# Performance work log

Hardware: AMD Instinct MI355X
Metric: run time of the kernel (lower is better)

## Reference

```python
import jax
import jax.numpy as jnp
import numpy as np

EPS = 1e-06


def _topk_mask(scores, k):
    # scores: (T, E); hard top-k mask along last dim
    _, idx = jax.lax.top_k(scores, k)            # (T, k)
    hard = jax.nn.one_hot(idx, scores.shape[-1]).sum(axis=-2)  # (T, E)
    return hard.astype(bool)


def setup_inputs() -> dict:
    key = jax.random.key(0)
    k1, k2, k3 = jax.random.split(key, 3)
    T, D, E = 8192, 4096, 64
    h_td = jax.random.normal(k1, (T, D), dtype=jnp.float32)
    # eqx.nn.Linear weight layout: (out_features, in_features)
    W = jax.random.normal(k2, (E, D), dtype=jnp.float32) * (1.0 / np.sqrt(D))
    bias_e = jax.random.normal(k3, (E,), dtype=jnp.float32)
    return {"h_td": h_td, "W": W, "bias_e": bias_e, "k": 8}


def reference(h_td, W, bias_e, k):
    # Linear(d_model -> E), no bias in proj; external bias_e added after
    logits_te = jnp.einsum("td,ed->te", h_td, W) + bias_e[None, :]  # (T, E)
    # Soft combine weights always from clean logits
    weight_te = jax.nn.softmax(logits_te, axis=-1)
    # Training path: Gumbel noise on the selection scores only
    gkey = jax.random.key(42)
    u = jax.random.uniform(gkey, logits_te.shape, minval=EPS, maxval=1.0 - EPS)
    g = -jnp.log(-jnp.log(u))
    sel_scores = logits_te + g
    mask_te = _topk_mask(sel_scores, k)
    return (mask_te, weight_te, logits_te)
```

## Files before the change

### kernel.cpp

```cpp
#include <hip/hip_runtime.h>
#include <stdint.h>
#include <math.h>

#define T_DIM 8192
#define D_DIM 4096
#define E_DIM 64
#define TE (T_DIM * E_DIM)
#define GAP_MARGIN 4e-3
#define BK 256
#define NCHUNK (D_DIM / BK)
#define KSTEPS (BK / 32)

typedef __attribute__((ext_vector_type(8))) short short8_t;
typedef __attribute__((ext_vector_type(4))) float f32x4;

__device__ __forceinline__ void threefry2x32_k42(uint32_t x0, uint32_t x1,
                                                 uint32_t& o0, uint32_t& o1) {
  const uint32_t ks0 = 0u, ks1 = 42u;
  const uint32_t ks2 = 0x1BD11BDAu ^ ks0 ^ ks1;
  x0 += ks0; x1 += ks1;
#define TF_RND(r) { x0 += x1; x1 = (x1 << (r)) | (x1 >> (32 - (r))); x1 ^= x0; }
  TF_RND(13) TF_RND(15) TF_RND(26) TF_RND(6)   x0 += ks1; x1 += ks2 + 1u;
  TF_RND(17) TF_RND(29) TF_RND(16) TF_RND(24)  x0 += ks2; x1 += ks0 + 2u;
  TF_RND(13) TF_RND(15) TF_RND(26) TF_RND(6)   x0 += ks0; x1 += ks1 + 3u;
  TF_RND(17) TF_RND(29) TF_RND(16) TF_RND(24)  x0 += ks1; x1 += ks2 + 4u;
  TF_RND(13) TF_RND(15) TF_RND(26) TF_RND(6)   x0 += ks2; x1 += ks0 + 5u;
#undef TF_RND
  o0 = x0; o1 = x1;
}

__device__ __forceinline__ uint32_t jax_random_bits32(uint32_t j) {
  uint32_t o0, o1;
  threefry2x32_k42(0u, j, o0, o1);
  return o0 ^ o1;
}

__device__ __forceinline__ void finalize_row_f64(double logit, int e, int t,
                                                 float& mask_out, float& weight_out,
                                                 double& gap_out) {
  double m = logit;
#pragma unroll
  for (int off = 1; off < 64; off <<= 1) {
    const double om = __shfl_xor(m, off, 64);
    m = (om > m) ? om : m;
  }
  const double pe = exp(logit - m);
  double s = pe;
#pragma unroll
  for (int off = 1; off < 64; off <<= 1) s += __shfl_xor(s, off, 64);
  weight_out = (float)(pe / s);

  const int idx = t * 64 + e;
  const uint32_t bits = jax_random_bits32((uint32_t)idx);
  const float f01 = __uint_as_float((bits >> 9) | 0x3f800000u) - 1.0f;
  const float minv = 1e-6f;
  const float maxv = 0.999999f;
  float u = __fadd_rn(__fmul_rn(f01, maxv - minv), minv);
  u = fmaxf(minv, u);
  const double g = -log(-log((double)u));
  const double sel = logit + g;

  float mask = 0.0f;
  double cur = sel;
  double v8 = 0.0, v9 = 0.0;
  for (int it = 0; it < 9; ++it) {
    double v = cur;
    int vi = e;
#pragma unroll
    for (int off = 1; off < 64; off <<= 1) {
      const double ov = __shfl_xor(v, off, 64);
      const int    oi = __shfl_xor(vi, off, 64);
      if (ov > v || (ov == v && oi < vi)) { v = ov; vi = oi; }
    }
    if (it < 8) {
      if (vi == e) { mask = 1.0f; cur = -__builtin_inf(); }
      if (it == 7) v8 = v;
    } else {
      v9 = v;
    }
  }
  mask_out = mask;
  gap_out = v8 - v9;
}

__device__ __forceinline__ uint16_t f2bf(float f) {
  const uint32_t x = __float_as_uint(f);
  return (uint16_t)((x + 0x7FFFu + ((x >> 16) & 1u)) >> 16);
}

__device__ __forceinline__ void split_write4(short* hiP, short* loP, float4 v) {
  ushort4 hi, lo;
  float fh;
  hi.x = f2bf(v.x); fh = __uint_as_float((uint32_t)hi.x << 16); lo.x = f2bf(v.x - fh);
  hi.y = f2bf(v.y); fh = __uint_as_float((uint32_t)hi.y << 16); lo.y = f2bf(v.y - fh);
  hi.z = f2bf(v.z); fh = __uint_as_float((uint32_t)hi.z << 16); lo.z = f2bf(v.z - fh);
  hi.w = f2bf(v.w); fh = __uint_as_float((uint32_t)hi.w << 16); lo.w = f2bf(v.w - fh);
  *reinterpret_cast<ushort4*>(hiP) = hi;
  *reinterpret_cast<ushort4*>(loP) = lo;
}

__global__ __launch_bounds__(512)
void router_mfma_kernel(const float* __restrict__ h,
                        const float* __restrict__ W,
                        const float* __restrict__ bias,
                        float* __restrict__ out,
                        unsigned char* __restrict__ flags) {
  __shared__ short Ahi[KSTEPS * 1024];
  __shared__ short Alo[KSTEPS * 1024];
  __shared__ short Bhi[KSTEPS * 2048];
  __shared__ short Blo[KSTEPS * 2048];
  __shared__ float logits_lds[32 * 65];

  const int tid   = threadIdx.x;
  const int wave  = tid >> 6;
  const int lane  = tid & 63;
  const int m_sub = wave & 1;
  const int n_sub = wave >> 1;
  const int row0  = blockIdx.x * 32;

  f32x4 acc = {0.0f, 0.0f, 0.0f, 0.0f};

  float4 pa[4];
  float4 pb[8];

#pragma unroll
  for (int s4 = 0; s4 < 4; ++s4) {
    const int flat = (tid + 512 * s4) * 4;
    const int r = flat >> 8, c = flat & 255;
    pa[s4] = *reinterpret_cast<const float4*>(h + (size_t)(row0 + r) * D_DIM + c);
  }
#pragma unroll
  for (int s8 = 0; s8 < 8; ++s8) {
    const int flat = (tid + 512 * s8) * 4;
    const int e = flat >> 8, k = flat & 255;
    pb[s8] = *reinterpret_cast<const float4*>(W + (size_t)e * D_DIM + k);
  }

  for (int chunk = 0; chunk < NCHUNK; ++chunk) {
#pragma unroll
    for (int s4 = 0; s4 < 4; ++s4) {
      const int flat = (tid + 512 * s4) * 4;
      const int r = flat >> 8, c = flat & 255;
      const int s = c >> 5, q = (c >> 3) & 3, j = c & 7;
      const int idx = s * 1024 + (r >> 4) * 512 + (q * 16 + (r & 15)) * 8 + j;
      split_write4(&Ahi[idx], &Alo[idx], pa[s4]);
    }
#pragma unroll
    for (int s8 = 0; s8 < 8; ++s8) {
      const int flat = (tid + 512 * s8) * 4;
      const int e = flat >> 8, k = flat & 255;
      const int s = k >> 5, q = (k >> 3) & 3, j = k & 7;
      const int idx = s * 2048 + (e >> 4) * 512 + (q * 16 + (e & 15)) * 8 + j;
      split_write4(&Bhi[idx], &Blo[idx], pb[s8]);
    }
    __syncthreads();

    if (chunk + 1 < NCHUNK) {
      const int kc = (chunk + 1) * BK;
#pragma unroll
      for (int s4 = 0; s4 < 4; ++s4) {
        const int flat = (tid + 512 * s4) * 4;
        const int r = flat >> 8, c = flat & 255;
        pa[s4] = *reinterpret_cast<const float4*>(h + (size_t)(row0 + r) * D_DIM + kc + c);
      }
#pragma unroll
      for (int s8 = 0; s8 < 8; ++s8) {
        const int flat = (tid + 512 * s8) * 4;
        const int e = flat >> 8, k = flat & 255;
        pb[s8] = *reinterpret_cast<const float4*>(W + (size_t)e * D_DIM + kc + k);
      }
    }

    const int aoff = m_sub * 512 + lane * 8;
    const int boff = n_sub * 512 + lane * 8;
#pragma unroll
    for (int s = 0; s < KSTEPS; ++s) {
      const short8_t ah = *reinterpret_cast<const short8_t*>(&Ahi[s * 1024 + aoff]);
      const short8_t al = *reinterpret_cast<const short8_t*>(&Alo[s * 1024 + aoff]);
      const short8_t bh = *reinterpret_cast<const short8_t*>(&Bhi[s * 2048 + boff]);
      const short8_t bl = *reinterpret_cast<const short8_t*>(&Blo[s * 2048 + boff]);
      acc = __builtin_amdgcn_mfma_f32_16x16x32_bf16(al, bh, acc, 0, 0, 0);
      acc = __builtin_amdgcn_mfma_f32_16x16x32_bf16(ah, bl, acc, 0, 0, 0);
      acc = __builtin_amdgcn_mfma_f32_16x16x32_bf16(ah, bh, acc, 0, 0, 0);
    }
    __syncthreads();
  }

  {
    const int q   = lane >> 4;
    const int col = n_sub * 16 + (lane & 15);
#pragma unroll
    for (int reg = 0; reg < 4; ++reg) {
      const int m = m_sub * 16 + q * 4 + reg;
      logits_lds[m * 65 + col] = acc[reg];
    }
  }
  __syncthreads();

  const int e = lane;
  const double be = (double)bias[e];
  for (int rr = 0; rr < 4; ++rr) {
    const int rloc = wave * 4 + rr;
    const int t = row0 + rloc;
    const double logit = (double)logits_lds[rloc * 65 + e] + be;

    float mask, weight;
    double gap;
    finalize_row_f64(logit, e, t, mask, weight, gap);

    const int idx = t * 64 + e;
    out[idx]          = mask;
    out[TE + idx]     = weight;
    out[2 * TE + idx] = (float)logit;
    if (e == 0) flags[t] = (gap < GAP_MARGIN) ? 1 : 0;
  }
}

__global__ __launch_bounds__(256)
void router_fixup_kernel(const float* __restrict__ h,
                         const float* __restrict__ W,
                         const float* __restrict__ bias,
                         const unsigned char* __restrict__ flags,
                         float* __restrict__ out) {
  const int t = blockIdx.x;
  if (flags[t] == 0) return;

  __shared__ double red[4][64];

  const int tid  = threadIdx.x;
  const int wv   = tid >> 6;
  const int lane = tid & 63;

  const float* hrow = h + (size_t)t * D_DIM + wv * 1024;

  float hv[16];
#pragma unroll
  for (int j = 0; j < 16; ++j) hv[j] = hrow[j * 64 + lane];

  for (int e = 0; e < 64; ++e) {
    const float* wrow = W + (size_t)e * D_DIM + wv * 1024;
    double a = 0.0;
#pragma unroll
    for (int j = 0; j < 16; ++j) {
      a = fma((double)wrow[j * 64 + lane], (double)hv[j], a);
    }
#pragma unroll
    for (int off = 1; off < 64; off <<= 1) a += __shfl_xor(a, off, 64);
    if (lane == e) red[wv][e] = a;
  }
  __syncthreads();

  if (wv == 0) {
    const int e = lane;
    const double logit = ((red[0][e] + red[1][e]) + (red[2][e] + red[3][e]))
                         + (double)bias[e];
    float mask, weight;
    double gap;
    finalize_row_f64(logit, e, t, mask, weight, gap);

    const int idx = t * 64 + e;
    out[idx]          = mask;
    out[TE + idx]     = weight;
    out[2 * TE + idx] = (float)logit;
  }
}

extern "C" void kernel_launch(void* const* d_in, const int* in_sizes, int n_in,
                              void* d_out, int out_size, void* d_ws, size_t ws_size,
                              hipStream_t stream) {
  const float* h    = (const float*)d_in[0];
  const float* W    = (const float*)d_in[1];
  const float* bias = (const float*)d_in[2];
  float* out = (float*)d_out;
  unsigned char* flags = (unsigned char*)d_ws;

  router_mfma_kernel<<<T_DIM / 32, 512, 0, stream>>>(h, W, bias, out, flags);
  router_fixup_kernel<<<T_DIM, 256, 0, stream>>>(h, W, bias, flags, out);
}
```

Baseline: 320.2 us.

## Pre-split W to bf16 hi/lo once, shrink row tile and double-buffer A

A new kernel converts W once per call into bf16 hi/lo pairs stored in global memory, already in MFMA fragment layout. The main kernel then reads B fragments straight from global/L2 instead of re-splitting W into LDS in every block. The main kernel now uses 16-row tiles with 256 threads, BK=128, a double-buffered A tile with an XOR swizzle, and one barrier per chunk. The fixup kernel is unrolled over 4 experts at a time to increase ILP. The costs are an extra launch and B traffic that now hits L2 on every k-step rather than LDS.

```diff
diff --git a/kernel.cpp b/kernel.cpp
--- a/kernel.cpp
+++ b/kernel.cpp
@@ -7,12 +7,16 @@
 #define E_DIM 64
 #define TE (T_DIM * E_DIM)
 #define GAP_MARGIN 4e-3
-#define BK 256
+#define BK 128
 #define NCHUNK (D_DIM / BK)
 #define KSTEPS (BK / 32)
+#define ROWS 16
 
 typedef __attribute__((ext_vector_type(8))) short short8_t;
 typedef __attribute__((ext_vector_type(4))) float f32x4;
+
+__device__ __align__(16) short Whi_g[E_DIM * D_DIM];
+__device__ __align__(16) short Wlo_g[E_DIM * D_DIM];
 
 __device__ __forceinline__ void threefry2x32_k42(uint32_t x0, uint32_t x1,
                                                  uint32_t& o0, uint32_t& o1) {
@@ -88,110 +92,106 @@
   return (uint16_t)((x + 0x7FFFu + ((x >> 16) & 1u)) >> 16);
 }
 
-__device__ __forceinline__ void split_write4(short* hiP, short* loP, float4 v) {
-  ushort4 hi, lo;
-  float fh;
-  hi.x = f2bf(v.x); fh = __uint_as_float((uint32_t)hi.x << 16); lo.x = f2bf(v.x - fh);
-  hi.y = f2bf(v.y); fh = __uint_as_float((uint32_t)hi.y << 16); lo.y = f2bf(v.y - fh);
-  hi.z = f2bf(v.z); fh = __uint_as_float((uint32_t)hi.z << 16); lo.z = f2bf(v.z - fh);
-  hi.w = f2bf(v.w); fh = __uint_as_float((uint32_t)hi.w << 16); lo.w = f2bf(v.w - fh);
-  *reinterpret_cast<ushort4*>(hiP) = hi;
-  *reinterpret_cast<ushort4*>(loP) = lo;
-}
-
-__global__ __launch_bounds__(512)
+__device__ __forceinline__ void split8(const float4 a, const float4 b,
+                                       short8_t& hi, short8_t& lo) {
+  const float f[8] = {a.x, a.y, a.z, a.w, b.x, b.y, b.z, b.w};
+#pragma unroll
+  for (int j = 0; j < 8; ++j) {
+    const uint16_t hb = f2bf(f[j]);
+    const float fh = __uint_as_float((uint32_t)hb << 16);
+    const uint16_t lb = f2bf(f[j] - fh);
+    hi[j] = (short)hb;
+    lo[j] = (short)lb;
+  }
+}
+
+__global__ __launch_bounds__(256)
+void w_split_kernel(const float* __restrict__ W) {
+  const int g = blockIdx.x * 256 + threadIdx.x;
+#pragma unroll
+  for (int r = 0; r < 2; ++r) {
+    const int u = g * 2 + r;
+    const int e = u >> 9;
+    const int k0 = (u & 511) * 8;
+    const float* wp = W + (size_t)e * D_DIM + k0;
+    const float4 a = *reinterpret_cast<const float4*>(wp);
+    const float4 b = *reinterpret_cast<const float4*>(wp + 4);
+    short8_t hi, lo;
+    split8(a, b, hi, lo);
+    const int ch = k0 >> 7, s = (k0 >> 5) & 3, q = (k0 >> 3) & 3;
+    const int subE = e >> 4, ee = e & 15;
+    const int idx = ch * 8192 + s * 2048 + subE * 512 + q * 128 + ee * 8;
+    *reinterpret_cast<short8_t*>(Whi_g + idx) = hi;
+    *reinterpret_cast<short8_t*>(Wlo_g + idx) = lo;
+  }
+}
+
+__global__ __launch_bounds__(256, 2)
 void router_mfma_kernel(const float* __restrict__ h,
-                        const float* __restrict__ W,
                         const float* __restrict__ bias,
                         float* __restrict__ out,
                         unsigned char* __restrict__ flags) {
-  __shared__ short Ahi[KSTEPS * 1024];
-  __shared__ short Alo[KSTEPS * 1024];
-  __shared__ short Bhi[KSTEPS * 2048];
-  __shared__ short Blo[KSTEPS * 2048];
-  __shared__ float logits_lds[32 * 65];
-
-  const int tid   = threadIdx.x;
-  const int wave  = tid >> 6;
-  const int lane  = tid & 63;
-  const int m_sub = wave & 1;
-  const int n_sub = wave >> 1;
-  const int row0  = blockIdx.x * 32;
+  __shared__ __align__(16) short Ahi[2][KSTEPS * 512];
+  __shared__ __align__(16) short Alo[2][KSTEPS * 512];
+  __shared__ float logits_lds[ROWS * 65];
+
+  const int tid  = threadIdx.x;
+  const int wave = tid >> 6;
+  const int lane = tid & 63;
+  const int row0 = blockIdx.x * ROWS;
+
+  const int a_row  = tid >> 4;
+  const int a_koct = tid & 15;
+  const int a_s = a_koct >> 2, a_q = a_koct & 3;
+  const int u_w0 = a_s * 64 + a_q * 16 + a_row;
+  const int u_w  = u_w0 ^ ((u_w0 >> 4) & 7);
+  const int a_widx = u_w * 8;
+  const float* hrow = h + (size_t)(row0 + a_row) * D_DIM + a_koct * 8;
+
+  const int b_off = wave * 512 + (lane >> 4) * 128 + (lane & 15) * 8;
 
   f32x4 acc = {0.0f, 0.0f, 0.0f, 0.0f};
 
-  float4 pa[4];
-  float4 pb[8];
-
-#pragma unroll
-  for (int s4 = 0; s4 < 4; ++s4) {
-    const int flat = (tid + 512 * s4) * 4;
-    const int r = flat >> 8, c = flat & 255;
-    pa[s4] = *reinterpret_cast<const float4*>(h + (size_t)(row0 + r) * D_DIM + c);
-  }
-#pragma unroll
-  for (int s8 = 0; s8 < 8; ++s8) {
-    const int flat = (tid + 512 * s8) * 4;
-    const int e = flat >> 8, k = flat & 255;
-    pb[s8] = *reinterpret_cast<const float4*>(W + (size_t)e * D_DIM + k);
-  }
-
-  for (int chunk = 0; chunk < NCHUNK; ++chunk) {
-#pragma unroll
-    for (int s4 = 0; s4 < 4; ++s4) {
-      const int flat = (tid + 512 * s4) * 4;
-      const int r = flat >> 8, c = flat & 255;
-      const int s = c >> 5, q = (c >> 3) & 3, j = c & 7;
-      const int idx = s * 1024 + (r >> 4) * 512 + (q * 16 + (r & 15)) * 8 + j;
-      split_write4(&Ahi[idx], &Alo[idx], pa[s4]);
-    }
-#pragma unroll
-    for (int s8 = 0; s8 < 8; ++s8) {
-      const int flat = (tid + 512 * s8) * 4;
-      const int e = flat >> 8, k = flat & 255;
-      const int s = k >> 5, q = (k >> 3) & 3, j = k & 7;
-      const int idx = s * 2048 + (e >> 4) * 512 + (q * 16 + (e & 15)) * 8 + j;
-      split_write4(&Bhi[idx], &Blo[idx], pb[s8]);
-    }
+  float4 pa0 = *reinterpret_cast<const float4*>(hrow);
+  float4 pa1 = *reinterpret_cast<const float4*>(hrow + 4);
+
+  int buf = 0;
+  for (int ch = 0; ch < NCHUNK; ++ch) {
+    short8_t hi, lo;
+    split8(pa0, pa1, hi, lo);
+    *reinterpret_cast<short8_t*>(&Ahi[buf][a_widx]) = hi;
+    *reinterpret_cast<short8_t*>(&Alo[buf][a_widx]) = lo;
     __syncthreads();
 
-    if (chunk + 1 < NCHUNK) {
-      const int kc = (chunk + 1) * BK;
-#pragma unroll
-      for (int s4 = 0; s4 < 4; ++s4) {
-        const int flat = (tid + 512 * s4) * 4;
-        const int r = flat >> 8, c = flat & 255;
-        pa[s4] = *reinterpret_cast<const float4*>(h + (size_t)(row0 + r) * D_DIM + kc + c);
-      }
-#pragma unroll
-      for (int s8 = 0; s8 < 8; ++s8) {
-        const int flat = (tid + 512 * s8) * 4;
-        const int e = flat >> 8, k = flat & 255;
-        pb[s8] = *reinterpret_cast<const float4*>(W + (size_t)e * D_DIM + kc + k);
-      }
-    }
-
-    const int aoff = m_sub * 512 + lane * 8;
-    const int boff = n_sub * 512 + lane * 8;
+    if (ch + 1 < NCHUNK) {
+      const float* p = hrow + (size_t)(ch + 1) * BK;
+      pa0 = *reinterpret_cast<const float4*>(p);
+      pa1 = *reinterpret_cast<const float4*>(p + 4);
+    }
+
+    const short* bhp = Whi_g + (size_t)ch * 8192 + b_off;
+    const short* blp = Wlo_g + (size_t)ch * 8192 + b_off;
 #pragma unroll
     for (int s = 0; s < KSTEPS; ++s) {
-      const short8_t ah = *reinterpret_cast<const short8_t*>(&Ahi[s * 1024 + aoff]);
-      const short8_t al = *reinterpret_cast<const short8_t*>(&Alo[s * 1024 + aoff]);
-      const short8_t bh = *reinterpret_cast<const short8_t*>(&Bhi[s * 2048 + boff]);
-      const short8_t bl = *reinterpret_cast<const short8_t*>(&Blo[s * 2048 + boff]);
+      const int ur0 = s * 64 + lane;
+      const int ur  = ur0 ^ ((ur0 >> 4) & 7);
+      const short8_t ah = *reinterpret_cast<const short8_t*>(&Ahi[buf][ur * 8]);
+      const short8_t al = *reinterpret_cast<const short8_t*>(&Alo[buf][ur * 8]);
+      const short8_t bh = *reinterpret_cast<const short8_t*>(bhp + s * 2048);
+      const short8_t bl = *reinterpret_cast<const short8_t*>(blp + s * 2048);
       acc = __builtin_amdgcn_mfma_f32_16x16x32_bf16(al, bh, acc, 0, 0, 0);
       acc = __builtin_amdgcn_mfma_f32_16x16x32_bf16(ah, bl, acc, 0, 0, 0);
       acc = __builtin_amdgcn_mfma_f32_16x16x32_bf16(ah, bh, acc, 0, 0, 0);
     }
-    __syncthreads();
+    buf ^= 1;
   }
 
   {
     const int q   = lane >> 4;
-    const int col = n_sub * 16 + (lane & 15);
+    const int col = wave * 16 + (lane & 15);
 #pragma unroll
     for (int reg = 0; reg < 4; ++reg) {
-      const int m = m_sub * 16 + q * 4 + reg;
+      const int m = q * 4 + reg;
       logits_lds[m * 65 + col] = acc[reg];
     }
   }
@@ -237,16 +237,31 @@
 #pragma unroll
   for (int j = 0; j < 16; ++j) hv[j] = hrow[j * 64 + lane];
 
-  for (int e = 0; e < 64; ++e) {
-    const float* wrow = W + (size_t)e * D_DIM + wv * 1024;
-    double a = 0.0;
+  for (int e0 = 0; e0 < 64; e0 += 4) {
+    const float* w0 = W + (size_t)(e0 + 0) * D_DIM + wv * 1024;
+    const float* w1 = W + (size_t)(e0 + 1) * D_DIM + wv * 1024;
+    const float* w2 = W + (size_t)(e0 + 2) * D_DIM + wv * 1024;
+    const float* w3 = W + (size_t)(e0 + 3) * D_DIM + wv * 1024;
+    double a0 = 0.0, a1 = 0.0, a2 = 0.0, a3 = 0.0;
 #pragma unroll
     for (int j = 0; j < 16; ++j) {
-      a = fma((double)wrow[j * 64 + lane], (double)hv[j], a);
-    }
-#pragma unroll
-    for (int off = 1; off < 64; off <<= 1) a += __shfl_xor(a, off, 64);
-    if (lane == e) red[wv][e] = a;
+      const double hd = (double)hv[j];
+      a0 = fma((double)w0[j * 64 + lane], hd, a0);
+      a1 = fma((double)w1[j * 64 + lane], hd, a1);
+      a2 = fma((double)w2[j * 64 + lane], hd, a2);
+      a3 = fma((double)w3[j * 64 + lane], hd, a3);
+    }
+#pragma unroll
+    for (int off = 1; off < 64; off <<= 1) {
+      a0 += __shfl_xor(a0, off, 64);
+      a1 += __shfl_xor(a1, off, 64);
+      a2 += __shfl_xor(a2, off, 64);
+      a3 += __shfl_xor(a3, off, 64);
+    }
+    if (lane == e0 + 0) red[wv][lane] = a0;
+    if (lane == e0 + 1) red[wv][lane] = a1;
+    if (lane == e0 + 2) red[wv][lane] = a2;
+    if (lane == e0 + 3) red[wv][lane] = a3;
   }
   __syncthreads();
 
@@ -274,6 +289,7 @@
   float* out = (float*)d_out;
   unsigned char* flags = (unsigned char*)d_ws;
 
-  router_mfma_kernel<<<T_DIM / 32, 512, 0, stream>>>(h, W, bias, out, flags);
+  w_split_kernel<<<64, 256, 0, stream>>>(W);
+  router_mfma_kernel<<<T_DIM / ROWS, 256, 0, stream>>>(h, bias, out, flags);
   router_fixup_kernel<<<T_DIM, 256, 0, stream>>>(h, W, bias, flags, out);
 }
```

Result: faster. 293.8 us (-8.2%).
